# Performance work log

Hardware: AMD Instinct MI355X
Metric: run time of the kernel (lower is better)

Reference implementation:

```python
import jax, jax.numpy as jnp
import numpy as np

B, C, W, H = 4, 256, 64, 64
K = C // 8      # key_channels = in_channels // 8
O = C           # out_channels = in_channels


def setup_inputs() -> dict:
    key = jax.random.key(0)
    ks = jax.random.split(key, 8)
    x = jax.random.normal(ks[0], (B, C, W, H), dtype=jnp.float32)
    # 1x1 conv weights stored as [out, in]; conv-style fan-in init scale
    s = 1.0 / np.sqrt(C)
    Wq = jax.random.uniform(ks[1], (K, C), minval=-s, maxval=s, dtype=jnp.float32)
    bq = jax.random.uniform(ks[2], (K,), minval=-s, maxval=s, dtype=jnp.float32)
    Wk = jax.random.uniform(ks[3], (K, C), minval=-s, maxval=s, dtype=jnp.float32)
    bk = jax.random.uniform(ks[4], (K,), minval=-s, maxval=s, dtype=jnp.float32)
    Wv = jax.random.uniform(ks[5], (O, C), minval=-s, maxval=s, dtype=jnp.float32)
    bv = jax.random.uniform(ks[6], (O,), minval=-s, maxval=s, dtype=jnp.float32)
    # gamma is zero-init in the module; use a small nonzero value so the
    # attention branch contributes measurably (kernel-testing baseline)
    gamma = 0.1 * jax.random.normal(ks[7], (1,), dtype=jnp.float32)
    return {"x": x, "Wq": Wq, "bq": bq, "Wk": Wk, "bk": bk,
            "Wv": Wv, "bv": bv, "gamma": gamma}


def reference(x, Wq, bq, Wk, bk, Wv, bv, gamma):
    b, c, w, h = x.shape
    n = w * h
    xr = x.reshape(b, c, n)                                   # B,C,N
    # 1x1 convs == per-pixel linear projections
    q = jnp.einsum('kc,bcn->bnk', Wq, xr) + bq                # B,N,K (permuted query)
    k = jnp.einsum('kc,bcn->bkn', Wk, xr) + bk[:, None]       # B,K,N
    energy = jnp.einsum('bnk,bkm->bnm', q, k)                 # B,N,N
    attention = jax.nn.softmax(energy, axis=-1)
    v = jnp.einsum('oc,bcn->bon', Wv, xr) + bv[:, None]       # B,O,N
    # out = bmm(V, attention^T): out[b,o,m] = sum_n V[b,o,n] * attn[b,m,n]
    out = jnp.einsum('bon,bmn->bom', v, attention)
    out = out.reshape(b, O, w, h)
    out = gamma * out + x                                     # true skip connection
    return out, attention
```

## Files before the change

### kernel.cpp

```cpp
#include <hip/hip_runtime.h>

#define NB  4
#define CCH 256
#define NN  4096
#define KD  32
#define OD  256

typedef __attribute__((ext_vector_type(8))) __bf16 bf16x8;
typedef __attribute__((ext_vector_type(4))) float  floatx4;

__device__ __forceinline__ unsigned short f2bf(float f) {
    union { float f; unsigned u; } v; v.f = f;
    unsigned r = v.u + 0x7FFFu + ((v.u >> 16) & 1u);
    return (unsigned short)(r >> 16);
}
__device__ __forceinline__ float bf2f(unsigned short h) {
    union { unsigned u; float f; } v; v.u = ((unsigned)h) << 16;
    return v.f;
}
__device__ __forceinline__ bf16x8 ldfrag(const unsigned short* p) {
    union { bf16x8 v; unsigned u[4]; } r;
    r.u[0] = *(const unsigned*)(p + 0);
    r.u[1] = *(const unsigned*)(p + 2);
    r.u[2] = *(const unsigned*)(p + 4);
    r.u[3] = *(const unsigned*)(p + 6);
    return r.v;
}

#define WPAD 66
#define VPAD 136

__global__ __launch_bounds__(256) void proj_kernel(
    const float* __restrict__ x,
    const float* __restrict__ Wq, const float* __restrict__ bq,
    const float* __restrict__ Wk, const float* __restrict__ bk,
    const float* __restrict__ Wv, const float* __restrict__ bv,
    unsigned short* __restrict__ Qb, unsigned short* __restrict__ Ktb,
    unsigned short* __restrict__ Vb)
{
    __shared__ __align__(16) unsigned char smem[50944];
    unsigned short* Wh   = (unsigned short*)smem;
    unsigned short* Wl   = (unsigned short*)(smem + 8448);
    unsigned short* Xth  = (unsigned short*)(smem + 16896);
    unsigned short* Xtl  = (unsigned short*)(smem + 33792);
    float*          bias = (float*)(smem + 50688);
    unsigned short* Yt = (unsigned short*)(smem + 16896);
    unsigned short* Vt = (unsigned short*)(smem + 16896);

    const int bid = blockIdx.x;
    const int mc  = bid >> 7;
    const int pnl = bid & 127;
    const int nb  = pnl & 31;
    const int b   = pnl >> 5;

    const int tid = threadIdx.x;
    const int wave = tid >> 6;
    const int lane = tid & 63;
    const int quad = lane >> 4;
    const int li   = lane & 15;
    const int pxw  = wave * 32;
    const int px0  = nb * 128;

    const float* xb = x + (size_t)b * CCH * NN;

    floatx4 acc[4][2];
    #pragma unroll
    for (int mf = 0; mf < 4; ++mf)
        #pragma unroll
        for (int nf = 0; nf < 2; ++nf)
            acc[mf][nf] = (floatx4){0.f, 0.f, 0.f, 0.f};

    for (int ks = 0; ks < 4; ++ks) {
        const int c0 = ks * 64;
        __syncthreads();

        #pragma unroll
        for (int i = 0; i < 4; ++i) {
            int idx4 = i * 256 + tid;
            int row  = idx4 >> 4;
            int c4   = (idx4 & 15) * 4;
            const float* src;
            if (mc == 0) src = (row < 32) ? (Wq + row * CCH) : (Wk + (row - 32) * CCH);
            else         src = Wv + ((size_t)((mc - 1) * 64 + row)) * CCH;
            floatx4 w = *(const floatx4*)(src + c0 + c4);
            #pragma unroll
            for (int j = 0; j < 4; ++j) {
                unsigned short h = f2bf(w[j]);
                unsigned short l = f2bf(w[j] - bf2f(h));
                Wh[row * WPAD + c4 + j] = h;
                Wl[row * WPAD + c4 + j] = l;
            }
        }
        #pragma unroll
        for (int i = 0; i < 8; ++i) {
            int idx4 = i * 256 + tid;
            int c    = idx4 >> 5;
            int px   = (idx4 & 31) * 4;
            floatx4 v = *(const floatx4*)(xb + (size_t)(c0 + c) * NN + px0 + px);
            #pragma unroll
            for (int j = 0; j < 4; ++j) {
                unsigned short h = f2bf(v[j]);
                unsigned short l = f2bf(v[j] - bf2f(h));
                Xth[(px + j) * WPAD + c] = h;
                Xtl[(px + j) * WPAD + c] = l;
            }
        }
        if (ks == 0 && tid < 64) {
            float bb;
            if (mc == 0) bb = (tid < 32) ? bq[tid] : bk[tid - 32];
            else         bb = bv[(mc - 1) * 64 + tid];
            bias[tid] = bb;
        }
        __syncthreads();

        #pragma unroll
        for (int kk = 0; kk < 2; ++kk) {
            bf16x8 ah[4], al[4], bh[2], bl[2];
            #pragma unroll
            for (int mf = 0; mf < 4; ++mf) {
                const int ro = (mf * 16 + li) * WPAD + kk * 32 + quad * 8;
                ah[mf] = ldfrag(Wh + ro);
                al[mf] = ldfrag(Wl + ro);
            }
            #pragma unroll
            for (int nf = 0; nf < 2; ++nf) {
                const int ro = (pxw + nf * 16 + li) * WPAD + kk * 32 + quad * 8;
                bh[nf] = ldfrag(Xth + ro);
                bl[nf] = ldfrag(Xtl + ro);
            }
            #pragma unroll
            for (int mf = 0; mf < 4; ++mf)
                #pragma unroll
                for (int nf = 0; nf < 2; ++nf) {
                    acc[mf][nf] = __builtin_amdgcn_mfma_f32_16x16x32_bf16(ah[mf], bh[nf], acc[mf][nf], 0, 0, 0);
                    acc[mf][nf] = __builtin_amdgcn_mfma_f32_16x16x32_bf16(ah[mf], bl[nf], acc[mf][nf], 0, 0, 0);
                    acc[mf][nf] = __builtin_amdgcn_mfma_f32_16x16x32_bf16(al[mf], bh[nf], acc[mf][nf], 0, 0, 0);
                }
        }
    }

    __syncthreads();
    if (mc == 0) {
        #pragma unroll
        for (int mf = 0; mf < 4; ++mf)
            #pragma unroll
            for (int nf = 0; nf < 2; ++nf)
                #pragma unroll
                for (int r = 0; r < 4; ++r) {
                    const int o = mf * 16 + quad * 4 + r;
                    float f = acc[mf][nf][r] + bias[o];
                    Yt[(pxw + nf * 16 + li) * WPAD + o] = f2bf(f);
                }
        __syncthreads();
        if (tid < 128) {
            const int px = tid;
            const size_t n = (size_t)(b * NN + px0 + px);
            unsigned short* qdst = Qb  + n * KD;
            unsigned short* kdst = Ktb + n * KD;
            const unsigned short* src = Yt + px * WPAD;
            #pragma unroll
            for (int i = 0; i < 4; ++i) {
                union { uint4 u4; unsigned u[4]; } q, k;
                #pragma unroll
                for (int j = 0; j < 4; ++j) {
                    q.u[j] = *(const unsigned*)(src + i * 8 + j * 2);
                    k.u[j] = *(const unsigned*)(src + 32 + i * 8 + j * 2);
                }
                *(uint4*)(qdst + i * 8) = q.u4;
                *(uint4*)(kdst + i * 8) = k.u4;
            }
        }
    } else {
        #pragma unroll
        for (int mf = 0; mf < 4; ++mf)
            #pragma unroll
            for (int nf = 0; nf < 2; ++nf)
                #pragma unroll
                for (int r = 0; r < 4; ++r) {
                    const int o = mf * 16 + quad * 4 + r;
                    float f = acc[mf][nf][r] + bias[o];
                    Vt[o * VPAD + pxw + nf * 16 + li] = f2bf(f);
                }
        __syncthreads();
        const int ol   = tid >> 2;
        const int part = tid & 3;
        const unsigned short* src = Vt + ol * VPAD + part * 32;
        unsigned short* dst = Vb + (size_t)(b * OD + (mc - 1) * 64 + ol) * NN + px0 + part * 32;
        *(uint4*)(dst + 0) = *(const uint4*)(src + 0);
        *(uint4*)(dst + 8) = *(const uint4*)(src + 8);
        *(uint4*)(dst + 16) = *(const uint4*)(src + 16);
        *(uint4*)(dst + 24) = *(const uint4*)(src + 24);
    }
}

__global__ __launch_bounds__(256, 2) void attn_kernel(
    const float* __restrict__ x, const float* __restrict__ gammap,
    const unsigned short* __restrict__ Qb,
    const unsigned short* __restrict__ Ktb,
    const unsigned short* __restrict__ Vb,
    float* __restrict__ out, float* __restrict__ attn)
{
    __shared__ __align__(16) unsigned char smem[63744];
    unsigned short* Vlds  = (unsigned short*)smem;
    float*          panel = (float*)(smem + 40960);
    unsigned short* Pl    = (unsigned short*)(smem + 58368);
    float*          sred  = (float*)(smem + 63488);

    const int tid  = threadIdx.x;
    const int wave = tid >> 6;
    const int lane = tid & 63;
    const int quad = lane >> 4;
    const int li   = lane & 15;
    const int g    = wave & 1;
    const int h    = wave >> 1;

    const int bid = blockIdx.x;
    const int b   = (bid & 7) >> 1;
    const int mt  = ((bid >> 3) << 1) | (bid & 1);
    const int mw  = mt * 32;
    const int hb  = h * 2048;

    unsigned short* Vh   = Vlds + h * 10240;
    float*          pan  = panel + wave * 1088;
    unsigned short* Plds = Pl + wave * 640;

    const floatx4 zero = {0.f, 0.f, 0.f, 0.f};

    const bf16x8 aQ = *(const bf16x8*)(Qb + (size_t)(b * NN + mw + g * 16 + li) * KD + quad * 8);
    const unsigned short* ktbase = Ktb + (size_t)b * NN * KD + quad * 8;

    float lrow[4] = {0.f, 0.f, 0.f, 0.f};
    #pragma unroll 4
    for (int nt = 0; nt < 128; ++nt) {
        bf16x8 bK = *(const bf16x8*)(ktbase + (size_t)(hb + nt * 16 + li) * KD);
        floatx4 s = __builtin_amdgcn_mfma_f32_16x16x32_bf16(aQ, bK, zero, 0, 0, 0);
        #pragma unroll
        for (int r = 0; r < 4; ++r) lrow[r] += __expf(s[r]);
    }
    #pragma unroll
    for (int r = 0; r < 4; ++r) {
        #pragma unroll
        for (int xm = 1; xm < 16; xm <<= 1)
            lrow[r] += __shfl_xor(lrow[r], xm);
    }
    if (li == 0) {
        #pragma unroll
        for (int r = 0; r < 4; ++r) sred[(g * 2 + h) * 16 + quad * 4 + r] = lrow[r];
    }
    __syncthreads();
    float linv[4];
    #pragma unroll
    for (int r = 0; r < 4; ++r) {
        const int row = quad * 4 + r;
        linv[r] = 1.0f / (sred[(g * 2 + 0) * 16 + row] + sred[(g * 2 + 1) * 16 + row]);
    }

    floatx4 oacc[16];
    #pragma unroll
    for (int ot = 0; ot < 16; ++ot) oacc[ot] = zero;

    const int hs = tid >> 7;
    const int st = tid & 127;
    const unsigned short* vsrc = Vb + (size_t)b * OD * NN + hs * 2048;
    unsigned short*       vdst = Vlds + hs * 10240;

    bf16x8 vtmp[8];
    #pragma unroll
    for (int i = 0; i < 8; ++i) {
        int linear = i * 128 + st;
        int o = linear >> 2, p = linear & 3;
        vtmp[i] = *(const bf16x8*)(vsrc + (size_t)o * NN + p * 8);
    }

    for (int c = 0; c < 64; ++c) {
        const int n0 = hb + c * 32;

        __builtin_amdgcn_s_barrier();

        #pragma unroll
        for (int i = 0; i < 8; ++i) {
            int linear = i * 128 + st;
            int o = linear >> 2, p = linear & 3;
            *(bf16x8*)(vdst + o * 40 + p * 8) = vtmp[i];
        }
        asm volatile("s_waitcnt lgkmcnt(0)" ::: "memory");
        __builtin_amdgcn_s_barrier();

        bf16x8 bK0 = *(const bf16x8*)(ktbase + (size_t)(n0 + li) * KD);
        bf16x8 bK1 = *(const bf16x8*)(ktbase + (size_t)(n0 + 16 + li) * KD);

        if (c < 63) {
            #pragma unroll
            for (int i = 0; i < 8; ++i) {
                int linear = i * 128 + st;
                int o = linear >> 2, p = linear & 3;
                vtmp[i] = *(const bf16x8*)(vsrc + (size_t)o * NN + (c + 1) * 32 + p * 8);
            }
        }

        floatx4 s0 = __builtin_amdgcn_mfma_f32_16x16x32_bf16(aQ, bK0, zero, 0, 0, 0);
        floatx4 s1 = __builtin_amdgcn_mfma_f32_16x16x32_bf16(aQ, bK1, zero, 0, 0, 0);
        const int cc = c & 1;
        #pragma unroll
        for (int r = 0; r < 4; ++r) {
            float p0 = __expf(s0[r]) * linv[r];
            float p1 = __expf(s1[r]) * linv[r];
            const int row = quad * 4 + r;
            pan[row * 68 + cc * 32 + li]      = p0;
            pan[row * 68 + cc * 32 + 16 + li] = p1;
            Plds[row * 40 + li]      = f2bf(p0);
            Plds[row * 40 + 16 + li] = f2bf(p1);
        }
        bf16x8 aP = *(const bf16x8*)(Plds + li * 40 + quad * 8);
        #pragma unroll
        for (int ot = 0; ot < 16; ++ot) {
            bf16x8 bV = *(const bf16x8*)(Vh + (ot * 16 + li) * 40 + quad * 8);
            oacc[ot] = __builtin_amdgcn_mfma_f32_16x16x32_bf16(aP, bV, oacc[ot], 0, 0, 0);
        }
        if (cc) {
            float* ab = attn + ((size_t)(b * NN + mw + g * 16)) * NN + hb + (c - 1) * 32;
            #pragma unroll
            for (int it = 0; it < 4; ++it) {
                int row = it * 4 + quad;
                floatx4 v = *(const floatx4*)(pan + row * 68 + li * 4);
                *(floatx4*)(ab + (size_t)row * NN + li * 4) = v;
            }
        }
    }

    __syncthreads();
    float* Olds = (float*)(void*)smem;
    if (h == 0) {
        #pragma unroll
        for (int ot = 0; ot < 16; ++ot)
            #pragma unroll
            for (int r = 0; r < 4; ++r)
                Olds[(ot * 16 + li) * 36 + g * 16 + quad * 4 + r] = oacc[ot][r];
    }
    __syncthreads();
    if (h == 1) {
        #pragma unroll
        for (int ot = 0; ot < 16; ++ot)
            #pragma unroll
            for (int r = 0; r < 4; ++r)
                Olds[(ot * 16 + li) * 36 + g * 16 + quad * 4 + r] += oacc[ot][r];
    }
    __syncthreads();
    const float gm = gammap[0];
    #pragma unroll
    for (int it = 0; it < 8; ++it) {
        int linear = it * 256 + tid;
        int o = linear >> 3, seg = linear & 7;
        floatx4 ov = *(const floatx4*)(Olds + o * 36 + seg * 4);
        size_t gidx = (size_t)(b * OD + o) * NN + mw + seg * 4;
        floatx4 xv = *(const floatx4*)(x + gidx);
        floatx4 res;
        res[0] = gm * ov[0] + xv[0];
        res[1] = gm * ov[1] + xv[1];
        res[2] = gm * ov[2] + xv[2];
        res[3] = gm * ov[3] + xv[3];
        *(floatx4*)(out + gidx) = res;
    }
}

extern "C" void kernel_launch(void* const* d_in, const int* in_sizes, int n_in,
                              void* d_out, int out_size, void* d_ws, size_t ws_size,
                              hipStream_t stream) {
    const float* x     = (const float*)d_in[0];
    const float* Wq    = (const float*)d_in[1];
    const float* bq    = (const float*)d_in[2];
    const float* Wk    = (const float*)d_in[3];
    const float* bk    = (const float*)d_in[4];
    const float* Wv    = (const float*)d_in[5];
    const float* bv    = (const float*)d_in[6];
    const float* gamma = (const float*)d_in[7];

    float* out  = (float*)d_out;
    float* attn = out + (size_t)NB * OD * NN;

    unsigned short* Qb  = (unsigned short*)d_ws;
    unsigned short* Ktb = Qb  + (size_t)NB * NN * KD;
    unsigned short* Vb  = Ktb + (size_t)NB * NN * KD;

    proj_kernel<<<dim3(640), 256, 0, stream>>>(x, Wq, bq, Wk, bk, Wv, bv, Qb, Ktb, Vb);
    attn_kernel<<<dim3(512), 256, 0, stream>>>(x, gamma, Qb, Ktb, Vb, out, attn);
}
```

Measured before the change: 435.6 us.

## Double attention block size to share V tiles across more query rows

The attention kernel now runs 512 threads (8 waves) per block, each covering 64 query rows instead of 32, so every V chunk staged in LDS serves twice as many rows and global V traffic halves. The bf16 P staging buffer is dropped: probabilities are written once to a float panel and converted to bf16 when the MFMA A-fragment is read. K fragments are prefetched one iteration ahead, and attention rows are stored every chunk instead of every other chunk. The trade-offs are half as many blocks (256) on the GPU, higher register pressure at 512 threads with two blocks per CU requested, and extra barriers in the final two-pass reduction.

```diff
diff --git a/kernel.cpp b/kernel.cpp
--- a/kernel.cpp
+++ b/kernel.cpp
@@ -193,36 +193,34 @@
     }
 }
 
-__global__ __launch_bounds__(256, 2) void attn_kernel(
+__global__ __launch_bounds__(512, 2) void attn_kernel(
     const float* __restrict__ x, const float* __restrict__ gammap,
     const unsigned short* __restrict__ Qb,
     const unsigned short* __restrict__ Ktb,
     const unsigned short* __restrict__ Vb,
     float* __restrict__ out, float* __restrict__ attn)
 {
-    __shared__ __align__(16) unsigned char smem[63744];
+    __shared__ __align__(16) unsigned char smem[59904];
     unsigned short* Vlds  = (unsigned short*)smem;
     float*          panel = (float*)(smem + 40960);
-    unsigned short* Pl    = (unsigned short*)(smem + 58368);
-    float*          sred  = (float*)(smem + 63488);
+    float*          sred  = (float*)(smem + 59392);
 
     const int tid  = threadIdx.x;
     const int wave = tid >> 6;
     const int lane = tid & 63;
     const int quad = lane >> 4;
     const int li   = lane & 15;
-    const int g    = wave & 1;
-    const int h    = wave >> 1;
+    const int g    = wave & 3;
+    const int h    = wave >> 2;
 
     const int bid = blockIdx.x;
     const int b   = (bid & 7) >> 1;
     const int mt  = ((bid >> 3) << 1) | (bid & 1);
-    const int mw  = mt * 32;
+    const int mw  = mt * 64;
     const int hb  = h * 2048;
 
-    unsigned short* Vh   = Vlds + h * 10240;
-    float*          pan  = panel + wave * 1088;
-    unsigned short* Plds = Pl + wave * 640;
+    unsigned short* Vh  = Vlds + h * 10240;
+    float*          pan = panel + wave * 576;
 
     const floatx4 zero = {0.f, 0.f, 0.f, 0.f};
 
@@ -259,107 +257,122 @@
     #pragma unroll
     for (int ot = 0; ot < 16; ++ot) oacc[ot] = zero;
 
-    const int hs = tid >> 7;
-    const int st = tid & 127;
+    const int hs = tid >> 8;
+    const int st = tid & 255;
     const unsigned short* vsrc = Vb + (size_t)b * OD * NN + hs * 2048;
     unsigned short*       vdst = Vlds + hs * 10240;
 
-    bf16x8 vtmp[8];
+    bf16x8 vtmp[4];
     #pragma unroll
-    for (int i = 0; i < 8; ++i) {
-        int linear = i * 128 + st;
+    for (int i = 0; i < 4; ++i) {
+        int linear = i * 256 + st;
         int o = linear >> 2, p = linear & 3;
         vtmp[i] = *(const bf16x8*)(vsrc + (size_t)o * NN + p * 8);
     }
+    bf16x8 bK0 = *(const bf16x8*)(ktbase + (size_t)(hb + li) * KD);
+    bf16x8 bK1 = *(const bf16x8*)(ktbase + (size_t)(hb + 16 + li) * KD);
 
     for (int c = 0; c < 64; ++c) {
-        const int n0 = hb + c * 32;
-
         __builtin_amdgcn_s_barrier();
 
         #pragma unroll
-        for (int i = 0; i < 8; ++i) {
-            int linear = i * 128 + st;
+        for (int i = 0; i < 4; ++i) {
+            int linear = i * 256 + st;
             int o = linear >> 2, p = linear & 3;
             *(bf16x8*)(vdst + o * 40 + p * 8) = vtmp[i];
         }
         asm volatile("s_waitcnt lgkmcnt(0)" ::: "memory");
         __builtin_amdgcn_s_barrier();
 
-        bf16x8 bK0 = *(const bf16x8*)(ktbase + (size_t)(n0 + li) * KD);
-        bf16x8 bK1 = *(const bf16x8*)(ktbase + (size_t)(n0 + 16 + li) * KD);
-
+        floatx4 s0 = __builtin_amdgcn_mfma_f32_16x16x32_bf16(aQ, bK0, zero, 0, 0, 0);
+        floatx4 s1 = __builtin_amdgcn_mfma_f32_16x16x32_bf16(aQ, bK1, zero, 0, 0, 0);
+
+        bf16x8 nK0, nK1;
         if (c < 63) {
-            #pragma unroll
-            for (int i = 0; i < 8; ++i) {
-                int linear = i * 128 + st;
+            const int n1 = hb + (c + 1) * 32;
+            nK0 = *(const bf16x8*)(ktbase + (size_t)(n1 + li) * KD);
+            nK1 = *(const bf16x8*)(ktbase + (size_t)(n1 + 16 + li) * KD);
+            #pragma unroll
+            for (int i = 0; i < 4; ++i) {
+                int linear = i * 256 + st;
                 int o = linear >> 2, p = linear & 3;
                 vtmp[i] = *(const bf16x8*)(vsrc + (size_t)o * NN + (c + 1) * 32 + p * 8);
             }
         }
 
-        floatx4 s0 = __builtin_amdgcn_mfma_f32_16x16x32_bf16(aQ, bK0, zero, 0, 0, 0);
-        floatx4 s1 = __builtin_amdgcn_mfma_f32_16x16x32_bf16(aQ, bK1, zero, 0, 0, 0);
-        const int cc = c & 1;
         #pragma unroll
         for (int r = 0; r < 4; ++r) {
             float p0 = __expf(s0[r]) * linv[r];
             float p1 = __expf(s1[r]) * linv[r];
             const int row = quad * 4 + r;
-            pan[row * 68 + cc * 32 + li]      = p0;
-            pan[row * 68 + cc * 32 + 16 + li] = p1;
-            Plds[row * 40 + li]      = f2bf(p0);
-            Plds[row * 40 + 16 + li] = f2bf(p1);
-        }
-        bf16x8 aP = *(const bf16x8*)(Plds + li * 40 + quad * 8);
-        #pragma unroll
-        for (int ot = 0; ot < 16; ++ot) {
-            bf16x8 bV = *(const bf16x8*)(Vh + (ot * 16 + li) * 40 + quad * 8);
-            oacc[ot] = __builtin_amdgcn_mfma_f32_16x16x32_bf16(aP, bV, oacc[ot], 0, 0, 0);
-        }
-        if (cc) {
-            float* ab = attn + ((size_t)(b * NN + mw + g * 16)) * NN + hb + (c - 1) * 32;
-            #pragma unroll
-            for (int it = 0; it < 4; ++it) {
-                int row = it * 4 + quad;
-                floatx4 v = *(const floatx4*)(pan + row * 68 + li * 4);
-                *(floatx4*)(ab + (size_t)row * NN + li * 4) = v;
-            }
-        }
-    }
-
-    __syncthreads();
+            pan[row * 36 + li]      = p0;
+            pan[row * 36 + 16 + li] = p1;
+        }
+        {
+            const float* prow = pan + li * 36 + quad * 8;
+            floatx4 pa = *(const floatx4*)(prow);
+            floatx4 pb = *(const floatx4*)(prow + 4);
+            union { bf16x8 v; unsigned short s[8]; } ap;
+            #pragma unroll
+            for (int j = 0; j < 4; ++j) {
+                ap.s[j]     = f2bf(pa[j]);
+                ap.s[4 + j] = f2bf(pb[j]);
+            }
+            #pragma unroll
+            for (int ot = 0; ot < 16; ++ot) {
+                bf16x8 bV = *(const bf16x8*)(Vh + (ot * 16 + li) * 40 + quad * 8);
+                oacc[ot] = __builtin_amdgcn_mfma_f32_16x16x32_bf16(ap.v, bV, oacc[ot], 0, 0, 0);
+            }
+        }
+        {
+            float* ab = attn + ((size_t)(b * NN + mw + g * 16)) * NN + hb + c * 32;
+            #pragma unroll
+            for (int it = 0; it < 2; ++it) {
+                int row = it * 8 + (lane >> 3);
+                int c4  = (lane & 7) * 4;
+                floatx4 v = *(const floatx4*)(pan + row * 36 + c4);
+                *(floatx4*)(ab + (size_t)row * NN + c4) = v;
+            }
+        }
+        bK0 = bK1;
+        if (c < 63) { bK0 = nK0; bK1 = nK1; }
+    }
+
+    const float gm = gammap[0];
     float* Olds = (float*)(void*)smem;
-    if (h == 0) {
-        #pragma unroll
-        for (int ot = 0; ot < 16; ++ot)
-            #pragma unroll
-            for (int r = 0; r < 4; ++r)
-                Olds[(ot * 16 + li) * 36 + g * 16 + quad * 4 + r] = oacc[ot][r];
-    }
-    __syncthreads();
-    if (h == 1) {
-        #pragma unroll
-        for (int ot = 0; ot < 16; ++ot)
-            #pragma unroll
-            for (int r = 0; r < 4; ++r)
-                Olds[(ot * 16 + li) * 36 + g * 16 + quad * 4 + r] += oacc[ot][r];
-    }
-    __syncthreads();
-    const float gm = gammap[0];
-    #pragma unroll
-    for (int it = 0; it < 8; ++it) {
-        int linear = it * 256 + tid;
-        int o = linear >> 3, seg = linear & 7;
-        floatx4 ov = *(const floatx4*)(Olds + o * 36 + seg * 4);
-        size_t gidx = (size_t)(b * OD + o) * NN + mw + seg * 4;
-        floatx4 xv = *(const floatx4*)(x + gidx);
-        floatx4 res;
-        res[0] = gm * ov[0] + xv[0];
-        res[1] = gm * ov[1] + xv[1];
-        res[2] = gm * ov[2] + xv[2];
-        res[3] = gm * ov[3] + xv[3];
-        *(floatx4*)(out + gidx) = res;
+    #pragma unroll 1
+    for (int p = 0; p < 2; ++p) {
+        __syncthreads();
+        if (h == 0 && (g >> 1) == p) {
+            #pragma unroll
+            for (int ot = 0; ot < 16; ++ot)
+                #pragma unroll
+                for (int r = 0; r < 4; ++r)
+                    Olds[(ot * 16 + li) * 36 + (g & 1) * 16 + quad * 4 + r] = oacc[ot][r];
+        }
+        __syncthreads();
+        if (h == 1 && (g >> 1) == p) {
+            #pragma unroll
+            for (int ot = 0; ot < 16; ++ot)
+                #pragma unroll
+                for (int r = 0; r < 4; ++r)
+                    Olds[(ot * 16 + li) * 36 + (g & 1) * 16 + quad * 4 + r] += oacc[ot][r];
+        }
+        __syncthreads();
+        #pragma unroll
+        for (int it = 0; it < 4; ++it) {
+            int linear = it * 512 + tid;
+            int o = linear >> 3, seg = linear & 7;
+            floatx4 ov = *(const floatx4*)(Olds + o * 36 + seg * 4);
+            size_t gidx = (size_t)(b * OD + o) * NN + mw + p * 32 + seg * 4;
+            floatx4 xv = *(const floatx4*)(x + gidx);
+            floatx4 res;
+            res[0] = gm * ov[0] + xv[0];
+            res[1] = gm * ov[1] + xv[1];
+            res[2] = gm * ov[2] + xv[2];
+            res[3] = gm * ov[3] + xv[3];
+            *(floatx4*)(out + gidx) = res;
+        }
     }
 }
 
@@ -383,5 +396,5 @@
     unsigned short* Vb  = Ktb + (size_t)NB * NN * KD;
 
     proj_kernel<<<dim3(640), 256, 0, stream>>>(x, Wq, bq, Wk, bk, Wv, bv, Qb, Ktb, Vb);
-    attn_kernel<<<dim3(512), 256, 0, stream>>>(x, gamma, Qb, Ktb, Vb, out, attn);
-}
+    attn_kernel<<<dim3(256), 512, 0, stream>>>(x, gamma, Qb, Ktb, Vb, out, attn);
+}
```

Result: no change. 435.8 us, median of 2 (+0.1%).
